# Optimization experiments

Hardware: AMD Instinct MI355X
Metric: run time of the kernel (lower is better)

Reference implementation:

```python
import jax, jax.numpy as jnp
import numpy as np

D_MODEL = 192
D_INNER = 384          # expand * d_model
D_STATE = 64
NHEADS = 8             # d_inner / headdim
HEADDIM = 48
D_CONV = 4
CONV_DIM = D_INNER + 2 * D_STATE   # 512 (ngroups=1)
D_IN_PROJ = 2 * D_INNER + 2 * D_STATE + NHEADS  # 904
MIX = 32
EPS = 1e-5


def silu(v):
    return v * jax.nn.sigmoid(v)


def setup_inputs() -> dict:
    key = jax.random.key(0)
    ks = jax.random.split(key, 16)
    B, L, C = 4, 4096, 4
    x = jax.random.normal(ks[0], (B, L, C), jnp.float32)
    Wfc = jax.random.normal(ks[1], (C, D_MODEL), jnp.float32) * 0.3
    bfc = jnp.zeros((D_MODEL,), jnp.float32)
    W_in = jax.random.normal(ks[2], (D_MODEL, D_IN_PROJ), jnp.float32) * 0.02
    conv_w = jax.random.normal(ks[3], (D_CONV, 1, CONV_DIM), jnp.float32) * 0.2  # depthwise (W,I/g,O)
    conv_b = jnp.zeros((CONV_DIM,), jnp.float32)
    # dt_bias = inv_softplus(dt_init) with dt_init ~ U(1e-3, 0.1)
    dt_init = jax.random.uniform(ks[4], (NHEADS,), jnp.float32, 1e-3, 0.1)
    dt_bias = jnp.log(jnp.expm1(dt_init))
    A_log = jnp.log(jax.random.uniform(ks[5], (NHEADS,), jnp.float32, 1.0, 16.0))
    Dparam = jnp.ones((NHEADS,), jnp.float32)
    norm_w = jnp.ones((D_INNER,), jnp.float32)
    W_out = jax.random.normal(ks[6], (D_INNER, D_MODEL), jnp.float32) * 0.02
    W1 = jax.random.normal(ks[7], (D_MODEL, MIX), jnp.float32) * 0.05
    b1 = jnp.zeros((MIX,), jnp.float32)
    W2 = jax.random.normal(ks[8], (MIX, MIX), jnp.float32) * 0.1
    b2 = jnp.zeros((MIX,), jnp.float32)
    Wo = jax.random.normal(ks[9], (MIX, 1), jnp.float32) * 0.1
    bo = jnp.zeros((1,), jnp.float32)
    return {"x": x, "Wfc": Wfc, "bfc": bfc, "W_in": W_in, "conv_w": conv_w,
            "conv_b": conv_b, "dt_bias": dt_bias, "A_log": A_log, "Dparam": Dparam,
            "norm_w": norm_w, "W_out": W_out, "W1": W1, "b1": b1, "W2": W2,
            "b2": b2, "Wo": Wo, "bo": bo}


def _mamba2(h, W_in, conv_w, conv_b, dt_bias, A_log, Dparam, norm_w, W_out):
    B, L, _ = h.shape
    zxbcdt = h @ W_in                                    # (B,L,904)
    z = zxbcdt[..., :D_INNER]
    xBC = zxbcdt[..., D_INNER:D_INNER + CONV_DIM]
    dt = jax.nn.softplus(zxbcdt[..., -NHEADS:] + dt_bias)  # (B,L,H)
    # causal depthwise conv1d
    xBC = jnp.pad(xBC, ((0, 0), (D_CONV - 1, 0), (0, 0)))
    xBC = jax.lax.conv_general_dilated(
        xBC, conv_w, window_strides=(1,), padding="VALID",
        dimension_numbers=("NWC", "WIO", "NWC"), feature_group_count=CONV_DIM)
    xBC = silu(xBC + conv_b)                             # (B,L,512)
    xs = xBC[..., :D_INNER].reshape(B, L, NHEADS, HEADDIM)
    Bm = xBC[..., D_INNER:D_INNER + D_STATE]             # (B,L,N)
    Cm = xBC[..., D_INNER + D_STATE:]                    # (B,L,N)
    A = -jnp.exp(A_log)                                  # (H,)
    dA = jnp.exp(dt * A)                                 # (B,L,H)

    def step(hstate, inp):
        dA_t, dt_t, B_t, x_t, C_t = inp                  # (B,H),(B,H),(B,N),(B,H,P),(B,N)
        dBx_t = jnp.einsum("bh,bn,bhp->bhpn", dt_t, B_t, x_t)
        hstate = dA_t[:, :, None, None] * hstate + dBx_t  # (B,H,P,N)
        y_t = jnp.einsum("bhpn,bn->bhp", hstate, C_t)
        return hstate, y_t

    h0 = jnp.zeros((B, NHEADS, HEADDIM, D_STATE), h.dtype)
    xs_t = jnp.swapaxes(xs, 0, 1)
    _, ys = jax.lax.scan(step, h0, (jnp.swapaxes(dA, 0, 1), jnp.swapaxes(dt, 0, 1),
                                    jnp.swapaxes(Bm, 0, 1), xs_t, jnp.swapaxes(Cm, 0, 1)))
    y = jnp.swapaxes(ys, 0, 1) + Dparam[None, None, :, None] * xs  # (B,L,H,P)
    y = y.reshape(B, L, D_INNER)
    # gated RMSNorm: rmsnorm(y * silu(z)) * weight
    y = y * silu(z)
    y = y * jax.lax.rsqrt(jnp.mean(y * y, axis=-1, keepdims=True) + EPS) * norm_w
    return y @ W_out                                     # (B,L,d_model)


def reference(x, Wfc, bfc, W_in, conv_w, conv_b, dt_bias, A_log, Dparam,
              norm_w, W_out, W1, b1, W2, b2, Wo, bo):
    h = x @ Wfc + bfc                                    # input_fc
    h = _mamba2(h, W_in, conv_w, conv_b, dt_bias, A_log, Dparam, norm_w, W_out)
    m = jax.nn.relu(h @ W1 + b1)
    m = jax.nn.relu(m @ W2 + b2)                         # dropout = identity (eval)
    m = jnp.mean(m, axis=1)                              # pool over time
    angle = (m @ Wo + bo)[:, 0]
    return angle
```

## Files before the change

kernel.cpp:

```cpp
#include <hip/hip_runtime.h>
#include <math.h>


#define BDIM 4
#define LDIM 4096
#define BL (BDIM*LDIM)
#define QC 64
#define NC (LDIM/QC)
#define BH (BDIM*NH)
#define NH 8

#define OFF_W    0u
#define OFF_Z    3145728u
#define OFF_T    9437184u
#define OFF_XS   17825792u
#define OFF_BM   24117248u
#define OFF_CM   25165824u
#define OFF_DT   26214400u
#define OFF_LAC  26345472u
#define OFF_SP   26476544u
#define OFF_Y    32768000u
#define OFF_MACC 39059456u

typedef unsigned short ushort_t;
typedef __attribute__((ext_vector_type(8))) short bf16x8;
typedef __attribute__((ext_vector_type(4))) float f32x4;

__device__ __forceinline__ float sigmoidf_(float x){ return 1.0f/(1.0f+__expf(-x)); }
__device__ __forceinline__ ushort_t f2bf(float x){
  unsigned int u = __float_as_uint(x);
  u += 0x7fffu + ((u>>16)&1u);
  return (ushort_t)(u>>16);
}
__device__ __forceinline__ float bf2f(ushort_t h){
  return __uint_as_float(((unsigned int)h)<<16);
}

__global__ void k_prep(const float* __restrict__ Wfc, const float* __restrict__ bfc,
                       const float* __restrict__ W_in, const float* __restrict__ W_out,
                       const float* __restrict__ W1,
                       float* __restrict__ Weff, float* __restrict__ beff,
                       float* __restrict__ Weff2, float* __restrict__ macc){
  int blk = blockIdx.x, tid = threadIdx.x;
  if (blk < 4){
    int n = blk*256 + tid;
    if (n >= 904) return;
    float a0=0.f,a1=0.f,a2=0.f,a3=0.f,ab=0.f;
    for (int d=0; d<192; d++){
      float w = W_in[(size_t)d*904 + n];
      a0 = fmaf(Wfc[d], w, a0);
      a1 = fmaf(Wfc[192+d], w, a1);
      a2 = fmaf(Wfc[384+d], w, a2);
      a3 = fmaf(Wfc[576+d], w, a3);
      ab = fmaf(bfc[d], w, ab);
    }
    Weff[n] = a0; Weff[904+n] = a1; Weff[1808+n] = a2; Weff[2712+n] = a3;
    beff[n] = ab;
  } else {
    if (blk == 4 && tid < 128) macc[tid] = 0.f;
    int g = (blk-4)*256 + tid;
    int i = g>>5, j = g&31;
    float a = 0.f;
    for (int d=0; d<192; d++) a = fmaf(W_out[(size_t)i*192+d], W1[d*32+j], a);
    Weff2[g] = a;
  }
}

__global__ __launch_bounds__(256) void k_ipc(
    const float* __restrict__ x, const float* __restrict__ Weff,
    const float* __restrict__ beff, const float* __restrict__ conv_w,
    const float* __restrict__ conv_b, const float* __restrict__ dt_bias,
    float* __restrict__ xs, float* __restrict__ Bm, float* __restrict__ Cm,
    float* __restrict__ dtb){
  __shared__ float sx[4][4];
  int bl = blockIdx.x, tid = threadIdx.x;
  int l = bl & 4095, b = bl >> 12;
  if (tid < 16){
    int k = tid>>2, r = tid&3;
    int ll = l-3+k;
    sx[k][r] = (ll>=0) ? x[(size_t)(b*4096+ll)*4 + r] : 0.f;
  }
  __syncthreads();
  if (tid < 8){
    float raw = beff[896+tid];
    #pragma unroll
    for (int r=0;r<4;r++) raw = fmaf(sx[3][r], Weff[r*904+896+tid], raw);
    float xx = raw + dt_bias[tid];
    float dtv = (xx > 20.f) ? xx : log1pf(__expf(xx));
    dtb[(size_t)(b*8+tid)*4096 + l] = dtv;
  }
  #pragma unroll
  for (int half=0; half<2; half++){
    int c = tid + half*256;
    float w0 = Weff[384+c];
    float w1 = Weff[904+384+c];
    float w2 = Weff[1808+384+c];
    float w3 = Weff[2712+384+c];
    float bb = beff[384+c];
    float acc = conv_b[c];
    #pragma unroll
    for (int k=0;k<4;k++){
      int ll = l-3+k;
      float xv = bb;
      xv = fmaf(sx[k][0], w0, xv);
      xv = fmaf(sx[k][1], w1, xv);
      xv = fmaf(sx[k][2], w2, xv);
      xv = fmaf(sx[k][3], w3, xv);
      if (ll < 0) xv = 0.f;
      acc = fmaf(conv_w[k*512+c], xv, acc);
    }
    float v = acc * sigmoidf_(acc);
    if (c < 384){
      int hh = c / 48, p = c - hh*48;
      xs[(size_t)((b*8+hh)*4096 + l)*48 + p] = v;
    } else if (c < 448){
      Bm[(size_t)bl*64 + (c-384)] = v;
    } else {
      Cm[(size_t)bl*64 + (c-448)] = v;
    }
  }
}

__global__ __launch_bounds__(256) void k_phase1(
    const float* __restrict__ dtbuf, const float* __restrict__ Bm,
    const float* __restrict__ xs, const float* __restrict__ A_log,
    float* __restrict__ T, float* __restrict__ lac){
  __shared__ __align__(16) ushort_t sBh[64*72], sBl[64*72];
  __shared__ __align__(16) ushort_t sXh[48*72], sXl[48*72];
  __shared__ float sdt[64], sla[64], sw[64];
  int tid = threadIdx.x, blk = blockIdx.x;
  int bh = blk >> 6, k = blk & 63;
  int b = bh >> 3, hh = bh & 7;
  int t0 = k*64;
  int w = tid>>6, lane = tid&63, l15 = lane&15, quad = lane>>4;

  if (tid < 64) sdt[tid] = dtbuf[(size_t)bh*4096 + t0 + tid];
  __syncthreads();
  if (tid == 0){
    float eA = __expf(A_log[hh]);
    float cum = 0.f;
    for (int i=0;i<64;i++){ cum -= sdt[i]*eA; sla[i] = cum; }
  }
  __syncthreads();
  if (tid < 64){
    sw[tid] = __expf(sla[63]-sla[tid])*sdt[tid];
    lac[(size_t)blk*64 + tid] = sla[tid];
  }
  __syncthreads();
  {
    int s2 = (tid&31)*2, ng = (tid>>5)*8;
    const float* b0 = Bm + (size_t)(b*4096+t0+s2)*64 + ng;
    const float* b1 = b0 + 64;
    float w0 = sw[s2], w1 = sw[s2+1];
    float4 a0 = *(const float4*)b0, a1 = *(const float4*)(b0+4);
    float4 c0 = *(const float4*)b1, c1 = *(const float4*)(b1+4);
    float v0[8] = {a0.x,a0.y,a0.z,a0.w,a1.x,a1.y,a1.z,a1.w};
    float v1[8] = {c0.x,c0.y,c0.z,c0.w,c1.x,c1.y,c1.z,c1.w};
    #pragma unroll
    for (int c=0;c<8;c++){
      float f0 = v0[c]*w0, f1 = v1[c]*w1;
      ushort_t h0 = f2bf(f0), h1 = f2bf(f1);
      ushort_t l0 = f2bf(f0-bf2f(h0)), l1 = f2bf(f1-bf2f(h1));
      int o = (ng+c)*72 + s2;
      *(unsigned int*)&sBh[o] = (unsigned int)h0 | ((unsigned int)h1<<16);
      *(unsigned int*)&sBl[o] = (unsigned int)l0 | ((unsigned int)l1<<16);
    }
  }
  {
    int s2 = (tid>>3)*2, p0 = (tid&7)*6;
    const float* x0 = xs + (size_t)(bh*4096+t0+s2)*48 + p0;
    const float* x1 = x0 + 48;
    #pragma unroll
    for (int c=0;c<6;c++){
      float a0 = x0[c], a1 = x1[c];
      ushort_t h0 = f2bf(a0), h1 = f2bf(a1);
      ushort_t l0 = f2bf(a0-bf2f(h0)), l1 = f2bf(a1-bf2f(h1));
      int o = (p0+c)*72 + s2;
      *(unsigned int*)&sXh[o] = (unsigned int)h0 | ((unsigned int)h1<<16);
      *(unsigned int*)&sXl[o] = (unsigned int)l0 | ((unsigned int)l1<<16);
    }
  }
  __syncthreads();
  f32x4 acc[3];
  #pragma unroll
  for (int t=0;t<3;t++) acc[t] = (f32x4)(0.f);
  #pragma unroll
  for (int ks=0;ks<2;ks++){
    int bo = (w*16+l15)*72 + ks*32 + quad*8;
    bf16x8 bbh = *(bf16x8*)&sBh[bo];
    bf16x8 bbl = *(bf16x8*)&sBl[bo];
    #pragma unroll
    for (int pt=0;pt<3;pt++){
      int xo = (pt*16+l15)*72 + ks*32 + quad*8;
      bf16x8 xah = *(bf16x8*)&sXh[xo];
      bf16x8 xal = *(bf16x8*)&sXl[xo];
      acc[pt] = __builtin_amdgcn_mfma_f32_16x16x32_bf16(xah, bbh, acc[pt], 0,0,0);
      acc[pt] = __builtin_amdgcn_mfma_f32_16x16x32_bf16(xah, bbl, acc[pt], 0,0,0);
      acc[pt] = __builtin_amdgcn_mfma_f32_16x16x32_bf16(xal, bbh, acc[pt], 0,0,0);
    }
  }
  {
    float* dst = T + (size_t)blk*3072;
    #pragma unroll
    for (int pt=0;pt<3;pt++)
      #pragma unroll
      for (int r=0;r<4;r++)
        dst[(pt*16+quad*4+r)*64 + w*16 + l15] = acc[pt][r];
  }
}

__global__ __launch_bounds__(256) void k_phase2p(
    const float* __restrict__ T, const float* __restrict__ lac, float* __restrict__ Sp){
  __shared__ __align__(16) float sT[64*64];
  __shared__ __align__(16) float sW[64][68];
  __shared__ float sc[64];
  int tid = threadIdx.x;
  int bh = blockIdx.x, es = blockIdx.y;
  #pragma unroll
  for (int r=0;r<4;r++){
    int idx = tid + r*256;
    int row = idx>>4, c4 = (idx&15)*4;
    *(float4*)&sT[row*64 + c4] = *(const float4*)(T + (size_t)(bh*64+row)*3072 + es*64 + c4);
  }
  if (tid < 64) sc[tid] = __expf(lac[(size_t)(bh*64+tid)*64 + 63]);
  __syncthreads();
  if (tid < 64){
    int k = tid;
    float w = 1.f;
    for (int j=63; j>=0; --j){
      bool a = (j < k);
      sW[j][k] = a ? w : 0.f;
      if (a) w *= sc[j];
    }
  }
  __syncthreads();
  int k0 = (tid>>4)*4, e0 = (tid&15)*4;
  float acc[4][4];
  #pragma unroll
  for (int i=0;i<4;i++)
    #pragma unroll
    for (int j=0;j<4;j++) acc[i][j]=0.f;
  int jmax = k0+2; if (jmax > 62) jmax = 62;
  for (int j=0; j<=jmax; ++j){
    float wv[4], tv[4];
    *(float4*)wv = *(float4*)&sW[j][k0];
    *(float4*)tv = *(float4*)&sT[j*64 + e0];
    #pragma unroll
    for (int i=0;i<4;i++)
      #pragma unroll
      for (int e=0;e<4;e++) acc[i][e] = fmaf(wv[i], tv[e], acc[i][e]);
  }
  #pragma unroll
  for (int i=0;i<4;i++){
    float4 o; o.x=acc[i][0]; o.y=acc[i][1]; o.z=acc[i][2]; o.w=acc[i][3];
    *(float4*)(Sp + (size_t)(bh*64+k0+i)*3072 + es*64 + e0) = o;
  }
}

__global__ __launch_bounds__(256, 3) void k_phase3(
    const float* __restrict__ dtbuf, const float* __restrict__ lac,
    const float* __restrict__ Bm, const float* __restrict__ Cm,
    const float* __restrict__ xs, const float* __restrict__ Sp,
    const float* __restrict__ Dparam, float* __restrict__ y){
  __shared__ __align__(16) ushort_t sCh[64*72], sCl[64*72];
  __shared__ __align__(16) ushort_t sBh[64*72], sBl[64*72];
  __shared__ __align__(16) ushort_t sXh[48*72], sXl[48*72];
  __shared__ float sla[64], sdt[64];
  int tid = threadIdx.x, blk = blockIdx.x;
  int bh = blk>>6, k = blk&63, b = bh>>3, hh = bh&7, t0 = k*64;
  int w = tid>>6, lane = tid&63, l15 = lane&15, quad = lane>>4;

  if (tid < 64){
    sdt[tid] = dtbuf[(size_t)bh*4096 + t0 + tid];
    sla[tid] = lac[(size_t)blk*64 + tid];
  }
  {
    int row = tid>>2, ng = (tid&3)*16;
    const float* csrc = Cm + (size_t)(b*4096+t0+row)*64 + ng;
    const float* bsrc = Bm + (size_t)(b*4096+t0+row)*64 + ng;
    #pragma unroll
    for (int q=0;q<4;q++){
      float4 cv = *(const float4*)(csrc + q*4);
      float4 bv = *(const float4*)(bsrc + q*4);
      ushort4 chv, clv, bhv, blv;
      chv.x=f2bf(cv.x); chv.y=f2bf(cv.y); chv.z=f2bf(cv.z); chv.w=f2bf(cv.w);
      clv.x=f2bf(cv.x-bf2f(chv.x)); clv.y=f2bf(cv.y-bf2f(chv.y));
      clv.z=f2bf(cv.z-bf2f(chv.z)); clv.w=f2bf(cv.w-bf2f(chv.w));
      bhv.x=f2bf(bv.x); bhv.y=f2bf(bv.y); bhv.z=f2bf(bv.z); bhv.w=f2bf(bv.w);
      blv.x=f2bf(bv.x-bf2f(bhv.x)); blv.y=f2bf(bv.y-bf2f(bhv.y));
      blv.z=f2bf(bv.z-bf2f(bhv.z)); blv.w=f2bf(bv.w-bf2f(bhv.w));
      int o = row*72 + ng + q*4;
      *(ushort4*)&sCh[o] = chv; *(ushort4*)&sCl[o] = clv;
      *(ushort4*)&sBh[o] = bhv; *(ushort4*)&sBl[o] = blv;
    }
  }
  {
    int s2 = (tid>>3)*2, p0 = (tid&7)*6;
    const float* x0 = xs + (size_t)(bh*4096+t0+s2)*48 + p0;
    const float* x1 = x0 + 48;
    #pragma unroll
    for (int c=0;c<6;c++){
      float a0 = x0[c], a1 = x1[c];
      ushort_t h0 = f2bf(a0), h1 = f2bf(a1);
      ushort_t l0 = f2bf(a0-bf2f(h0)), l1 = f2bf(a1-bf2f(h1));
      int o = (p0+c)*72 + s2;
      *(unsigned int*)&sXh[o] = (unsigned int)h0 | ((unsigned int)h1<<16);
      *(unsigned int*)&sXl[o] = (unsigned int)l0 | ((unsigned int)l1<<16);
    }
  }
  __syncthreads();

  f32x4 gacc[4];
  #pragma unroll
  for (int t=0;t<4;t++) gacc[t] = (f32x4)(0.f);
  {
    bf16x8 cah[2], cal[2];
    #pragma unroll
    for (int ks=0;ks<2;ks++){
      int ao = (w*16+l15)*72 + ks*32 + quad*8;
      cah[ks] = *(bf16x8*)&sCh[ao];
      cal[ks] = *(bf16x8*)&sCl[ao];
    }
    for (int bs=0; bs<=w; ++bs){
      #pragma unroll
      for (int ks=0;ks<2;ks++){
        int bo = (bs*16+l15)*72 + ks*32 + quad*8;
        bf16x8 bhf = *(bf16x8*)&sBh[bo];
        bf16x8 blf = *(bf16x8*)&sBl[bo];
        gacc[bs] = __builtin_amdgcn_mfma_f32_16x16x32_bf16(cah[ks], bhf, gacc[bs], 0,0,0);
        gacc[bs] = __builtin_amdgcn_mfma_f32_16x16x32_bf16(cah[ks], blf, gacc[bs], 0,0,0);
        gacc[bs] = __builtin_amdgcn_mfma_f32_16x16x32_bf16(cal[ks], bhf, gacc[bs], 0,0,0);
      }
    }
  }
  __syncthreads();

  for (int bs=0; bs<=w; ++bs){
    #pragma unroll
    for (int r=0;r<4;r++){
      int i = w*16 + quad*4 + r;
      int s = bs*16 + l15;
      float v = 0.f;
      if (s <= i) v = gacc[bs][r] * __expf(sla[i]-sla[s]) * sdt[s];
      ushort_t hi = f2bf(v);
      sBh[i*72+s] = hi;
      sBl[i*72+s] = f2bf(v - bf2f(hi));
    }
  }
  if (w==0){
    #pragma unroll
    for (int r=0;r<4;r++){ sBh[(quad*4+r)*72 + 16+l15] = 0; sBl[(quad*4+r)*72 + 16+l15] = 0; }
  }
  if (w==2){
    #pragma unroll
    for (int r=0;r<4;r++){ sBh[(32+quad*4+r)*72 + 48+l15] = 0; sBl[(32+quad*4+r)*72 + 48+l15] = 0; }
  }
  __syncthreads();

  float4 spv[3][2][2];
  {
    const float* sp0 = Sp + (size_t)blk*3072;
    #pragma unroll
    for (int pt=0;pt<3;pt++)
      #pragma unroll
      for (int ks=0;ks<2;ks++){
        const float* p = sp0 + (pt*16+l15)*64 + ks*32 + quad*8;
        spv[pt][ks][0] = *(const float4*)(p);
        spv[pt][ks][1] = *(const float4*)(p+4);
      }
  }

  f32x4 accI[3], accA[3];
  #pragma unroll
  for (int t=0;t<3;t++){ accI[t] = (f32x4)(0.f); accA[t] = (f32x4)(0.f); }
  int nks = (w>=2) ? 2 : 1;
  for (int ks=0; ks<nks; ++ks){
    int go = (w*16+l15)*72 + ks*32 + quad*8;
    bf16x8 gbh = *(bf16x8*)&sBh[go];
    bf16x8 gbl = *(bf16x8*)&sBl[go];
    #pragma unroll
    for (int pt=0;pt<3;pt++){
      int xo = (pt*16+l15)*72 + ks*32 + quad*8;
      bf16x8 xah = *(bf16x8*)&sXh[xo];
      bf16x8 xal = *(bf16x8*)&sXl[xo];
      accI[pt] = __builtin_amdgcn_mfma_f32_16x16x32_bf16(xah, gbh, accI[pt], 0,0,0);
      accI[pt] = __builtin_amdgcn_mfma_f32_16x16x32_bf16(xah, gbl, accI[pt], 0,0,0);
      accI[pt] = __builtin_amdgcn_mfma_f32_16x16x32_bf16(xal, gbh, accI[pt], 0,0,0);
    }
  }
  #pragma unroll
  for (int ks=0; ks<2; ++ks){
    int co = (w*16+l15)*72 + ks*32 + quad*8;
    bf16x8 cbh = *(bf16x8*)&sCh[co];
    bf16x8 cbl = *(bf16x8*)&sCl[co];
    #pragma unroll
    for (int pt=0;pt<3;pt++){
      const float* vv = (const float*)&spv[pt][ks][0];
      bf16x8 pah, pal;
      #pragma unroll
      for (int c=0;c<8;c++){
        ushort_t hi = f2bf(vv[c]);
        pah[c] = (short)hi;
        pal[c] = (short)f2bf(vv[c] - bf2f(hi));
      }
      accA[pt] = __builtin_amdgcn_mfma_f32_16x16x32_bf16(pah, cbh, accA[pt], 0,0,0);
      accA[pt] = __builtin_amdgcn_mfma_f32_16x16x32_bf16(pah, cbl, accA[pt], 0,0,0);
      accA[pt] = __builtin_amdgcn_mfma_f32_16x16x32_bf16(pal, cbh, accA[pt], 0,0,0);
    }
  }
  {
    int i = w*16 + l15;
    float eli = __expf(sla[i]);
    float Dh = Dparam[hh];
    float* ybase = y + (size_t)(b*4096+t0+i)*384 + hh*48;
    #pragma unroll
    for (int pt=0;pt<3;pt++)
      #pragma unroll
      for (int r=0;r<4;r++){
        int p = pt*16 + quad*4 + r;
        float xf = bf2f(sXh[p*72 + i]) + bf2f(sXl[p*72 + i]);
        ybase[p] = accI[pt][r] + eli*accA[pt][r] + Dh*xf;
      }
  }
}

__global__ __launch_bounds__(256) void k_gate(
    const float* __restrict__ x, const float* __restrict__ Weff,
    const float* __restrict__ beff, const float* __restrict__ norm_w,
    const float* __restrict__ y, float* __restrict__ yn){
  int tid = threadIdx.x;
  int w = tid>>6, lane = tid&63;
  int e0 = lane*6;
  float W0[6],W1v[6],W2v[6],W3v[6],bv[6],nw[6];
  #pragma unroll
  for (int c=0;c<6;c++){
    int e = e0+c;
    W0[c]=Weff[e]; W1v[c]=Weff[904+e]; W2v[c]=Weff[1808+e]; W3v[c]=Weff[2712+e];
    bv[c]=beff[e]; nw[c]=norm_w[e];
  }
  #pragma unroll
  for (int t=0;t<4;t++){
    int bl = blockIdx.x*16 + w*4 + t;
    float4 xv = *(const float4*)(x + (size_t)bl*4);
    float g[6]; float ss = 0.f;
    #pragma unroll
    for (int c=0;c<6;c++){
      float zv = bv[c];
      zv = fmaf(xv.x, W0[c], zv);
      zv = fmaf(xv.y, W1v[c], zv);
      zv = fmaf(xv.z, W2v[c], zv);
      zv = fmaf(xv.w, W3v[c], zv);
      float yv = y[(size_t)bl*384 + e0 + c];
      float gg = yv * (zv * sigmoidf_(zv));
      g[c] = gg; ss += gg*gg;
    }
    #pragma unroll
    for (int off=32; off>0; off>>=1) ss += __shfl_xor(ss, off);
    float rms = rsqrtf(ss*(1.f/384.f) + 1e-5f);
    #pragma unroll
    for (int c=0;c<6;c++)
      yn[(size_t)bl*384 + e0 + c] = g[c]*rms*nw[c];
  }
}

__global__ __launch_bounds__(256) void k_mlp2(
    const float* __restrict__ yn, const float* __restrict__ Weff2,
    const float* __restrict__ b1, const float* __restrict__ W2,
    const float* __restrict__ b2, float* __restrict__ macc){
  __shared__ __align__(16) float sW[384][32];
  __shared__ __align__(16) float sm1[64][33];
  __shared__ __align__(16) float sW2[32][32];
  __shared__ __align__(16) float sm2[64][33];
  int tid = threadIdx.x;
  int tok0 = blockIdx.x*64;
  int b = tok0 >> 12;
  #pragma unroll
  for (int r=0;r<12;r++){
    int idx = tid + r*256;
    int row = idx>>3, c4 = (idx&7)*4;
    *(float4*)&sW[row][c4] = *(const float4*)(Weff2 + (size_t)idx*4);
  }
  {
    int row = tid>>3, c4 = (tid&7)*4;
    *(float4*)&sW2[row][c4] = *(const float4*)(W2 + row*32 + c4);
  }
  __syncthreads();
  {
    int tk = tid>>3, j0 = (tid&7)*4;
    float a0[4], a1[4];
    #pragma unroll
    for (int j=0;j<4;j++){ a0[j] = b1[j0+j]; a1[j] = a0[j]; }
    const float* y0 = yn + (size_t)(tok0+tk)*384;
    const float* y1 = yn + (size_t)(tok0+tk+32)*384;
    for (int k4=0;k4<96;k4++){
      float4 va = *(const float4*)(y0 + k4*4);
      float4 vb = *(const float4*)(y1 + k4*4);
      float w[4];
      *(float4*)w = *(float4*)&sW[k4*4+0][j0];
      #pragma unroll
      for (int j=0;j<4;j++){ a0[j] = fmaf(va.x, w[j], a0[j]); a1[j] = fmaf(vb.x, w[j], a1[j]); }
      *(float4*)w = *(float4*)&sW[k4*4+1][j0];
      #pragma unroll
      for (int j=0;j<4;j++){ a0[j] = fmaf(va.y, w[j], a0[j]); a1[j] = fmaf(vb.y, w[j], a1[j]); }
      *(float4*)w = *(float4*)&sW[k4*4+2][j0];
      #pragma unroll
      for (int j=0;j<4;j++){ a0[j] = fmaf(va.z, w[j], a0[j]); a1[j] = fmaf(vb.z, w[j], a1[j]); }
      *(float4*)w = *(float4*)&sW[k4*4+3][j0];
      #pragma unroll
      for (int j=0;j<4;j++){ a0[j] = fmaf(va.w, w[j], a0[j]); a1[j] = fmaf(vb.w, w[j], a1[j]); }
    }
    #pragma unroll
    for (int j=0;j<4;j++){
      sm1[tk][j0+j]    = fmaxf(a0[j], 0.f);
      sm1[tk+32][j0+j] = fmaxf(a1[j], 0.f);
    }
  }
  __syncthreads();
  {
    int tk = tid>>3, j0 = (tid&7)*4;
    float a0[4], a1[4];
    #pragma unroll
    for (int j=0;j<4;j++){ a0[j] = b2[j0+j]; a1[j] = a0[j]; }
    #pragma unroll
    for (int kk=0;kk<32;kk++){
      float va = sm1[tk][kk];
      float vb = sm1[tk+32][kk];
      float w[4]; *(float4*)w = *(float4*)&sW2[kk][j0];
      #pragma unroll
      for (int j=0;j<4;j++){ a0[j] = fmaf(va, w[j], a0[j]); a1[j] = fmaf(vb, w[j], a1[j]); }
    }
    #pragma unroll
    for (int j=0;j<4;j++){
      sm2[tk][j0+j]    = fmaxf(a0[j], 0.f);
      sm2[tk+32][j0+j] = fmaxf(a1[j], 0.f);
    }
  }
  __syncthreads();
  if (tid < 32){
    float t = 0.f;
    #pragma unroll
    for (int tok=0;tok<64;tok++) t += sm2[tok][tid];
    atomicAdd(&macc[b*32 + tid], t);
  }
}

__global__ void k_final(const float* __restrict__ macc, const float* __restrict__ Wo,
                        const float* __restrict__ bo, float* __restrict__ out){
  int tid = threadIdx.x;
  if (tid < 4){
    float acc = bo[0];
    #pragma unroll
    for (int j=0;j<32;j++) acc = fmaf(macc[tid*32+j]*(1.f/4096.f), Wo[j], acc);
    out[tid] = acc;
  }
}

extern "C" void kernel_launch(void* const* d_in, const int* in_sizes, int n_in,
                              void* d_out, int out_size, void* d_ws, size_t ws_size,
                              hipStream_t stream){
  const float* x      = (const float*)d_in[0];
  const float* Wfc    = (const float*)d_in[1];
  const float* bfc    = (const float*)d_in[2];
  const float* W_in   = (const float*)d_in[3];
  const float* conv_w = (const float*)d_in[4];
  const float* conv_b = (const float*)d_in[5];
  const float* dt_bias= (const float*)d_in[6];
  const float* A_log  = (const float*)d_in[7];
  const float* Dparam = (const float*)d_in[8];
  const float* norm_w = (const float*)d_in[9];
  const float* W_out  = (const float*)d_in[10];
  const float* W1     = (const float*)d_in[11];
  const float* b1     = (const float*)d_in[12];
  const float* W2     = (const float*)d_in[13];
  const float* b2     = (const float*)d_in[14];
  const float* Wo     = (const float*)d_in[15];
  const float* bo     = (const float*)d_in[16];
  float* ws  = (float*)d_ws;
  float* out = (float*)d_out;

  float* Weff  = ws + OFF_W;
  float* beff  = ws + OFF_W + 4096;
  float* Weff2 = ws + OFF_W + 8192;
  float* yn    = ws + OFF_Z;
  float* Tb    = ws + OFF_T;
  float* xsb   = ws + OFF_XS;
  float* Bmb   = ws + OFF_BM;
  float* Cmb   = ws + OFF_CM;
  float* dtb   = ws + OFF_DT;
  float* lacb  = ws + OFF_LAC;
  float* Spb   = ws + OFF_SP;
  float* yb    = ws + OFF_Y;
  float* macc  = ws + OFF_MACC;

  k_prep<<<dim3(52), dim3(256), 0, stream>>>(Wfc, bfc, W_in, W_out, W1,
                                             Weff, beff, Weff2, macc);
  k_ipc<<<dim3(BL), dim3(256), 0, stream>>>(x, Weff, beff, conv_w, conv_b,
                                            dt_bias, xsb, Bmb, Cmb, dtb);
  k_phase1<<<dim3(BH*NC), dim3(256), 0, stream>>>(dtb, Bmb, xsb, A_log, Tb, lacb);
  k_phase2p<<<dim3(BH,48), dim3(256), 0, stream>>>(Tb, lacb, Spb);
  k_phase3<<<dim3(BH*NC), dim3(256), 0, stream>>>(dtb, lacb, Bmb, Cmb, xsb, Spb, Dparam, yb);
  k_gate<<<dim3(BL/16), dim3(256), 0, stream>>>(x, Weff, beff, norm_w, yb, yn);
  k_mlp2<<<dim3(BL/64), dim3(256), 0, stream>>>(yn, Weff2, b1, W2, b2, macc);
  k_final<<<dim3(1), dim3(64), 0, stream>>>(macc, Wo, bo, out);
}
```

Measured before the change: 218.1 us.

## Store conv outputs as bf16 hi/lo pairs and keep y, yn in bf16

The conv kernel now writes xs, B and C as precomputed bf16 hi/lo splits, so phase1 and phase3 skip the per-block float-to-split conversion and copy the split data straight into shared memory. The intermediate y and normalized yn buffers are stored as plain bf16, which halves their memory traffic through the gate and MLP kernels. Phase1 also gains a minimum-occupancy launch bound. Total bytes for xs/B/C stay the same, and keeping y and yn in bf16 lowers accuracy before the RMSNorm and MLP stages.

```diff
diff --git a/kernel.cpp b/kernel.cpp
--- a/kernel.cpp
+++ b/kernel.cpp
@@ -70,7 +70,9 @@
     const float* __restrict__ x, const float* __restrict__ Weff,
     const float* __restrict__ beff, const float* __restrict__ conv_w,
     const float* __restrict__ conv_b, const float* __restrict__ dt_bias,
-    float* __restrict__ xs, float* __restrict__ Bm, float* __restrict__ Cm,
+    ushort_t* __restrict__ xs_h, ushort_t* __restrict__ xs_l,
+    ushort_t* __restrict__ Bm_h, ushort_t* __restrict__ Bm_l,
+    ushort_t* __restrict__ Cm_h, ushort_t* __restrict__ Cm_l,
     float* __restrict__ dtb){
   __shared__ float sx[4][4];
   int bl = blockIdx.x, tid = threadIdx.x;
@@ -110,20 +112,27 @@
       acc = fmaf(conv_w[k*512+c], xv, acc);
     }
     float v = acc * sigmoidf_(acc);
+    ushort_t hi = f2bf(v);
+    ushort_t lo = f2bf(v - bf2f(hi));
     if (c < 384){
       int hh = c / 48, p = c - hh*48;
-      xs[(size_t)((b*8+hh)*4096 + l)*48 + p] = v;
+      size_t idx = (size_t)((b*8+hh)*4096 + l)*48 + p;
+      xs_h[idx] = hi; xs_l[idx] = lo;
     } else if (c < 448){
-      Bm[(size_t)bl*64 + (c-384)] = v;
+      size_t idx = (size_t)bl*64 + (c-384);
+      Bm_h[idx] = hi; Bm_l[idx] = lo;
     } else {
-      Cm[(size_t)bl*64 + (c-448)] = v;
-    }
-  }
-}
-
-__global__ __launch_bounds__(256) void k_phase1(
-    const float* __restrict__ dtbuf, const float* __restrict__ Bm,
-    const float* __restrict__ xs, const float* __restrict__ A_log,
+      size_t idx = (size_t)bl*64 + (c-448);
+      Cm_h[idx] = hi; Cm_l[idx] = lo;
+    }
+  }
+}
+
+__global__ __launch_bounds__(256, 3) void k_phase1(
+    const float* __restrict__ dtbuf,
+    const ushort_t* __restrict__ Bm_h, const ushort_t* __restrict__ Bm_l,
+    const ushort_t* __restrict__ xs_h, const ushort_t* __restrict__ xs_l,
+    const float* __restrict__ A_log,
     float* __restrict__ T, float* __restrict__ lac){
   __shared__ __align__(16) ushort_t sBh[64*72], sBl[64*72];
   __shared__ __align__(16) ushort_t sXh[48*72], sXl[48*72];
@@ -149,35 +158,35 @@
   __syncthreads();
   {
     int s2 = (tid&31)*2, ng = (tid>>5)*8;
-    const float* b0 = Bm + (size_t)(b*4096+t0+s2)*64 + ng;
-    const float* b1 = b0 + 64;
+    size_t base0 = (size_t)(b*4096+t0+s2)*64 + ng;
+    ushort_t h0a[8], l0a[8], h1a[8], l1a[8];
+    *(uint4*)h0a = *(const uint4*)(Bm_h + base0);
+    *(uint4*)l0a = *(const uint4*)(Bm_l + base0);
+    *(uint4*)h1a = *(const uint4*)(Bm_h + base0 + 64);
+    *(uint4*)l1a = *(const uint4*)(Bm_l + base0 + 64);
     float w0 = sw[s2], w1 = sw[s2+1];
-    float4 a0 = *(const float4*)b0, a1 = *(const float4*)(b0+4);
-    float4 c0 = *(const float4*)b1, c1 = *(const float4*)(b1+4);
-    float v0[8] = {a0.x,a0.y,a0.z,a0.w,a1.x,a1.y,a1.z,a1.w};
-    float v1[8] = {c0.x,c0.y,c0.z,c0.w,c1.x,c1.y,c1.z,c1.w};
     #pragma unroll
     for (int c=0;c<8;c++){
-      float f0 = v0[c]*w0, f1 = v1[c]*w1;
+      float f0 = (bf2f(h0a[c]) + bf2f(l0a[c])) * w0;
+      float f1 = (bf2f(h1a[c]) + bf2f(l1a[c])) * w1;
       ushort_t h0 = f2bf(f0), h1 = f2bf(f1);
-      ushort_t l0 = f2bf(f0-bf2f(h0)), l1 = f2bf(f1-bf2f(h1));
+      ushort_t lo0 = f2bf(f0-bf2f(h0)), lo1 = f2bf(f1-bf2f(h1));
       int o = (ng+c)*72 + s2;
       *(unsigned int*)&sBh[o] = (unsigned int)h0 | ((unsigned int)h1<<16);
-      *(unsigned int*)&sBl[o] = (unsigned int)l0 | ((unsigned int)l1<<16);
+      *(unsigned int*)&sBl[o] = (unsigned int)lo0 | ((unsigned int)lo1<<16);
     }
   }
   {
     int s2 = (tid>>3)*2, p0 = (tid&7)*6;
-    const float* x0 = xs + (size_t)(bh*4096+t0+s2)*48 + p0;
-    const float* x1 = x0 + 48;
+    const ushort_t* xh0 = xs_h + (size_t)(bh*4096+t0+s2)*48 + p0;
+    const ushort_t* xl0 = xs_l + (size_t)(bh*4096+t0+s2)*48 + p0;
     #pragma unroll
     for (int c=0;c<6;c++){
-      float a0 = x0[c], a1 = x1[c];
-      ushort_t h0 = f2bf(a0), h1 = f2bf(a1);
-      ushort_t l0 = f2bf(a0-bf2f(h0)), l1 = f2bf(a1-bf2f(h1));
+      unsigned int hv = (unsigned int)xh0[c] | ((unsigned int)xh0[48+c]<<16);
+      unsigned int lv = (unsigned int)xl0[c] | ((unsigned int)xl0[48+c]<<16);
       int o = (p0+c)*72 + s2;
-      *(unsigned int*)&sXh[o] = (unsigned int)h0 | ((unsigned int)h1<<16);
-      *(unsigned int*)&sXl[o] = (unsigned int)l0 | ((unsigned int)l1<<16);
+      *(unsigned int*)&sXh[o] = hv;
+      *(unsigned int*)&sXl[o] = lv;
     }
   }
   __syncthreads();
@@ -259,9 +268,11 @@
 
 __global__ __launch_bounds__(256, 3) void k_phase3(
     const float* __restrict__ dtbuf, const float* __restrict__ lac,
-    const float* __restrict__ Bm, const float* __restrict__ Cm,
-    const float* __restrict__ xs, const float* __restrict__ Sp,
-    const float* __restrict__ Dparam, float* __restrict__ y){
+    const ushort_t* __restrict__ Bm_h, const ushort_t* __restrict__ Bm_l,
+    const ushort_t* __restrict__ Cm_h, const ushort_t* __restrict__ Cm_l,
+    const ushort_t* __restrict__ xs_h, const ushort_t* __restrict__ xs_l,
+    const float* __restrict__ Sp, const float* __restrict__ Dparam,
+    ushort_t* __restrict__ y16){
   __shared__ __align__(16) ushort_t sCh[64*72], sCl[64*72];
   __shared__ __align__(16) ushort_t sBh[64*72], sBl[64*72];
   __shared__ __align__(16) ushort_t sXh[48*72], sXl[48*72];
@@ -276,36 +287,28 @@
   }
   {
     int row = tid>>2, ng = (tid&3)*16;
-    const float* csrc = Cm + (size_t)(b*4096+t0+row)*64 + ng;
-    const float* bsrc = Bm + (size_t)(b*4096+t0+row)*64 + ng;
-    #pragma unroll
-    for (int q=0;q<4;q++){
-      float4 cv = *(const float4*)(csrc + q*4);
-      float4 bv = *(const float4*)(bsrc + q*4);
-      ushort4 chv, clv, bhv, blv;
-      chv.x=f2bf(cv.x); chv.y=f2bf(cv.y); chv.z=f2bf(cv.z); chv.w=f2bf(cv.w);
-      clv.x=f2bf(cv.x-bf2f(chv.x)); clv.y=f2bf(cv.y-bf2f(chv.y));
-      clv.z=f2bf(cv.z-bf2f(chv.z)); clv.w=f2bf(cv.w-bf2f(chv.w));
-      bhv.x=f2bf(bv.x); bhv.y=f2bf(bv.y); bhv.z=f2bf(bv.z); bhv.w=f2bf(bv.w);
-      blv.x=f2bf(bv.x-bf2f(bhv.x)); blv.y=f2bf(bv.y-bf2f(bhv.y));
-      blv.z=f2bf(bv.z-bf2f(bhv.z)); blv.w=f2bf(bv.w-bf2f(bhv.w));
-      int o = row*72 + ng + q*4;
-      *(ushort4*)&sCh[o] = chv; *(ushort4*)&sCl[o] = clv;
-      *(ushort4*)&sBh[o] = bhv; *(ushort4*)&sBl[o] = blv;
-    }
+    size_t gb = (size_t)(b*4096+t0+row)*64 + ng;
+    int o = row*72 + ng;
+    *(uint4*)&sCh[o]   = *(const uint4*)(Cm_h + gb);
+    *(uint4*)&sCh[o+8] = *(const uint4*)(Cm_h + gb + 8);
+    *(uint4*)&sCl[o]   = *(const uint4*)(Cm_l + gb);
+    *(uint4*)&sCl[o+8] = *(const uint4*)(Cm_l + gb + 8);
+    *(uint4*)&sBh[o]   = *(const uint4*)(Bm_h + gb);
+    *(uint4*)&sBh[o+8] = *(const uint4*)(Bm_h + gb + 8);
+    *(uint4*)&sBl[o]   = *(const uint4*)(Bm_l + gb);
+    *(uint4*)&sBl[o+8] = *(const uint4*)(Bm_l + gb + 8);
   }
   {
     int s2 = (tid>>3)*2, p0 = (tid&7)*6;
-    const float* x0 = xs + (size_t)(bh*4096+t0+s2)*48 + p0;
-    const float* x1 = x0 + 48;
+    const ushort_t* xh0 = xs_h + (size_t)(bh*4096+t0+s2)*48 + p0;
+    const ushort_t* xl0 = xs_l + (size_t)(bh*4096+t0+s2)*48 + p0;
     #pragma unroll
     for (int c=0;c<6;c++){
-      float a0 = x0[c], a1 = x1[c];
-      ushort_t h0 = f2bf(a0), h1 = f2bf(a1);
-      ushort_t l0 = f2bf(a0-bf2f(h0)), l1 = f2bf(a1-bf2f(h1));
+      unsigned int hv = (unsigned int)xh0[c] | ((unsigned int)xh0[48+c]<<16);
+      unsigned int lv = (unsigned int)xl0[c] | ((unsigned int)xl0[48+c]<<16);
       int o = (p0+c)*72 + s2;
-      *(unsigned int*)&sXh[o] = (unsigned int)h0 | ((unsigned int)h1<<16);
-      *(unsigned int*)&sXl[o] = (unsigned int)l0 | ((unsigned int)l1<<16);
+      *(unsigned int*)&sXh[o] = hv;
+      *(unsigned int*)&sXl[o] = lv;
     }
   }
   __syncthreads();
@@ -412,14 +415,14 @@
     int i = w*16 + l15;
     float eli = __expf(sla[i]);
     float Dh = Dparam[hh];
-    float* ybase = y + (size_t)(b*4096+t0+i)*384 + hh*48;
+    ushort_t* ybase = y16 + (size_t)(b*4096+t0+i)*384 + hh*48;
     #pragma unroll
     for (int pt=0;pt<3;pt++)
       #pragma unroll
       for (int r=0;r<4;r++){
         int p = pt*16 + quad*4 + r;
         float xf = bf2f(sXh[p*72 + i]) + bf2f(sXl[p*72 + i]);
-        ybase[p] = accI[pt][r] + eli*accA[pt][r] + Dh*xf;
+        ybase[p] = f2bf(accI[pt][r] + eli*accA[pt][r] + Dh*xf);
       }
   }
 }
@@ -427,7 +430,7 @@
 __global__ __launch_bounds__(256) void k_gate(
     const float* __restrict__ x, const float* __restrict__ Weff,
     const float* __restrict__ beff, const float* __restrict__ norm_w,
-    const float* __restrict__ y, float* __restrict__ yn){
+    const ushort_t* __restrict__ y16, ushort_t* __restrict__ yn16){
   int tid = threadIdx.x;
   int w = tid>>6, lane = tid&63;
   int e0 = lane*6;
@@ -450,7 +453,7 @@
       zv = fmaf(xv.y, W1v[c], zv);
       zv = fmaf(xv.z, W2v[c], zv);
       zv = fmaf(xv.w, W3v[c], zv);
-      float yv = y[(size_t)bl*384 + e0 + c];
+      float yv = bf2f(y16[(size_t)bl*384 + e0 + c]);
       float gg = yv * (zv * sigmoidf_(zv));
       g[c] = gg; ss += gg*gg;
     }
@@ -459,12 +462,12 @@
     float rms = rsqrtf(ss*(1.f/384.f) + 1e-5f);
     #pragma unroll
     for (int c=0;c<6;c++)
-      yn[(size_t)bl*384 + e0 + c] = g[c]*rms*nw[c];
+      yn16[(size_t)bl*384 + e0 + c] = f2bf(g[c]*rms*nw[c]);
   }
 }
 
 __global__ __launch_bounds__(256) void k_mlp2(
-    const float* __restrict__ yn, const float* __restrict__ Weff2,
+    const ushort_t* __restrict__ yn16, const float* __restrict__ Weff2,
     const float* __restrict__ b1, const float* __restrict__ W2,
     const float* __restrict__ b2, float* __restrict__ macc){
   __shared__ __align__(16) float sW[384][32];
@@ -490,24 +493,19 @@
     float a0[4], a1[4];
     #pragma unroll
     for (int j=0;j<4;j++){ a0[j] = b1[j0+j]; a1[j] = a0[j]; }
-    const float* y0 = yn + (size_t)(tok0+tk)*384;
-    const float* y1 = yn + (size_t)(tok0+tk+32)*384;
-    for (int k4=0;k4<96;k4++){
-      float4 va = *(const float4*)(y0 + k4*4);
-      float4 vb = *(const float4*)(y1 + k4*4);
-      float w[4];
-      *(float4*)w = *(float4*)&sW[k4*4+0][j0];
-      #pragma unroll
-      for (int j=0;j<4;j++){ a0[j] = fmaf(va.x, w[j], a0[j]); a1[j] = fmaf(vb.x, w[j], a1[j]); }
-      *(float4*)w = *(float4*)&sW[k4*4+1][j0];
-      #pragma unroll
-      for (int j=0;j<4;j++){ a0[j] = fmaf(va.y, w[j], a0[j]); a1[j] = fmaf(vb.y, w[j], a1[j]); }
-      *(float4*)w = *(float4*)&sW[k4*4+2][j0];
-      #pragma unroll
-      for (int j=0;j<4;j++){ a0[j] = fmaf(va.z, w[j], a0[j]); a1[j] = fmaf(vb.z, w[j], a1[j]); }
-      *(float4*)w = *(float4*)&sW[k4*4+3][j0];
-      #pragma unroll
-      for (int j=0;j<4;j++){ a0[j] = fmaf(va.w, w[j], a0[j]); a1[j] = fmaf(vb.w, w[j], a1[j]); }
+    const ushort_t* y0 = yn16 + (size_t)(tok0+tk)*384;
+    const ushort_t* y1 = yn16 + (size_t)(tok0+tk+32)*384;
+    for (int k8=0;k8<48;k8++){
+      ushort_t ua[8], ub[8];
+      *(uint4*)ua = *(const uint4*)(y0 + k8*8);
+      *(uint4*)ub = *(const uint4*)(y1 + k8*8);
+      #pragma unroll
+      for (int c=0;c<8;c++){
+        float va = bf2f(ua[c]), vb = bf2f(ub[c]);
+        float w[4]; *(float4*)w = *(float4*)&sW[k8*8+c][j0];
+        #pragma unroll
+        for (int j=0;j<4;j++){ a0[j] = fmaf(va, w[j], a0[j]); a1[j] = fmaf(vb, w[j], a1[j]); }
+      }
     }
     #pragma unroll
     for (int j=0;j<4;j++){
@@ -581,25 +579,32 @@
   float* Weff  = ws + OFF_W;
   float* beff  = ws + OFF_W + 4096;
   float* Weff2 = ws + OFF_W + 8192;
-  float* yn    = ws + OFF_Z;
+  ushort_t* yn16 = (ushort_t*)(ws + OFF_Z);
   float* Tb    = ws + OFF_T;
-  float* xsb   = ws + OFF_XS;
-  float* Bmb   = ws + OFF_BM;
-  float* Cmb   = ws + OFF_CM;
+  ushort_t* xs_h = (ushort_t*)(ws + OFF_XS);
+  ushort_t* xs_l = xs_h + 6291456u;
+  ushort_t* Bm_h = (ushort_t*)(ws + OFF_BM);
+  ushort_t* Bm_l = Bm_h + 1048576u;
+  ushort_t* Cm_h = (ushort_t*)(ws + OFF_CM);
+  ushort_t* Cm_l = Cm_h + 1048576u;
   float* dtb   = ws + OFF_DT;
   float* lacb  = ws + OFF_LAC;
   float* Spb   = ws + OFF_SP;
-  float* yb    = ws + OFF_Y;
+  ushort_t* y16 = (ushort_t*)(ws + OFF_Y);
   float* macc  = ws + OFF_MACC;
 
   k_prep<<<dim3(52), dim3(256), 0, stream>>>(Wfc, bfc, W_in, W_out, W1,
                                              Weff, beff, Weff2, macc);
   k_ipc<<<dim3(BL), dim3(256), 0, stream>>>(x, Weff, beff, conv_w, conv_b,
-                                            dt_bias, xsb, Bmb, Cmb, dtb);
-  k_phase1<<<dim3(BH*NC), dim3(256), 0, stream>>>(dtb, Bmb, xsb, A_log, Tb, lacb);
+                                            dt_bias, xs_h, xs_l, Bm_h, Bm_l,
+                                            Cm_h, Cm_l, dtb);
+  k_phase1<<<dim3(BH*NC), dim3(256), 0, stream>>>(dtb, Bm_h, Bm_l, xs_h, xs_l,
+                                                  A_log, Tb, lacb);
   k_phase2p<<<dim3(BH,48), dim3(256), 0, stream>>>(Tb, lacb, Spb);
-  k_phase3<<<dim3(BH*NC), dim3(256), 0, stream>>>(dtb, lacb, Bmb, Cmb, xsb, Spb, Dparam, yb);
-  k_gate<<<dim3(BL/16), dim3(256), 0, stream>>>(x, Weff, beff, norm_w, yb, yn);
-  k_mlp2<<<dim3(BL/64), dim3(256), 0, stream>>>(yn, Weff2, b1, W2, b2, macc);
+  k_phase3<<<dim3(BH*NC), dim3(256), 0, stream>>>(dtb, lacb, Bm_h, Bm_l,
+                                                  Cm_h, Cm_l, xs_h, xs_l,
+                                                  Spb, Dparam, y16);
+  k_gate<<<dim3(BL/16), dim3(256), 0, stream>>>(x, Weff, beff, norm_w, y16, yn16);
+  k_mlp2<<<dim3(BL/64), dim3(256), 0, stream>>>(yn16, Weff2, b1, W2, b2, macc);
   k_final<<<dim3(1), dim3(64), 0, stream>>>(macc, Wo, bo, out);
 }
```

Result: faster. 209.4 us (-4.0%).
